# Kernel tuning notes

Hardware: AMD Instinct MI355X
Metric: run time of the kernel (lower is better)

Reference implementation:

```python
import math
import jax, jax.numpy as jnp
import numpy as np

B, T, C, H = 2, 1024, 1024, 16
D = C // H
BASE_SCALE = 0.03125
ATTN_ALPHA_INIT, MLP_ALPHA_INIT = 0.05, 0.05


def sinusoidal_embeddings(n, d):
    pos = jnp.arange(n, dtype=jnp.float32)[:, None]
    div = jnp.exp(jnp.arange(0, d, 2, dtype=jnp.float32) * (-math.log(10000.0) / d))
    emb = jnp.zeros((n, d), dtype=jnp.float32)
    emb = emb.at[:, 0::2].set(jnp.sin(pos * div))
    emb = emb.at[:, 1::2].set(jnp.cos(pos * div))
    return emb


def apply_rope(pos, q):
    # pos: (T, D); q: (B, H, T, D). Faithful to source: returns only the rotated-scaled component.
    pos = pos[-q.shape[2]:]
    d = q.shape[-1]
    sin, cos = pos[:, : d // 2], pos[:, d // 2 :]
    q_rot = jnp.stack((-q[..., 1::2], q[..., ::2]), axis=-1)  # (B,H,T,D/2,2)
    sc = jnp.stack((cos, sin), axis=-1)  # (T, D/2, 2)
    return (q_rot * sc).reshape(q.shape)


def justnorm(x):
    return x / jnp.linalg.norm(x, axis=-1, keepdims=True)


def setup_inputs() -> dict:
    key = jax.random.key(0)
    ks = jax.random.split(key, 14)
    w = lambda k, shape: jax.random.normal(k, shape, jnp.float32) * 0.02
    return {
        "h": jax.random.normal(ks[0], (B, T, C), jnp.float32),
        "Wq": w(ks[1], (C, C)),
        "Wk": w(ks[2], (C, C)),
        "Wv": w(ks[3], (C, C)),
        "Wo": w(ks[4], (C, C)),
        "Wfc": w(ks[5], (8 * C, C)),
        "Wproj": w(ks[6], (C, 4 * C)),
        "sqk": BASE_SCALE * jnp.ones(C) + w(ks[7], (C,)) * 0.05,
        "suv": jnp.ones(8 * C) + w(ks[8], (8 * C,)) * 0.05,
        "attn_alpha": BASE_SCALE * jnp.ones(C) + w(ks[9], (C,)) * 0.05,
        "mlp_alpha": BASE_SCALE * jnp.ones(C) + w(ks[10], (C,)) * 0.05,
        "thr_c": 1.6 * jnp.ones(H) + w(ks[11], (H,)) * 0.5,
        "stp": 10.0 * jnp.ones(H),
    }


def reference(h, Wq, Wk, Wv, Wo, Wfc, Wproj, sqk, suv, attn_alpha, mlp_alpha, thr_c, stp):
    softmax_scale = math.sqrt(D)  # nGPT uses sqrt(head_dim) since q,k are unit-normalized

    # --- attention branch (no pre-norm in nGPT mode) ---
    q = (h @ Wq.T).reshape(B, T, H, D).transpose(0, 2, 1, 3)  # (B,H,T,D)
    k = (h @ Wk.T).reshape(B, T, H, D).transpose(0, 2, 1, 3)
    v = (h @ Wv.T).reshape(B, T, H, D).transpose(0, 2, 1, 3)

    pos = sinusoidal_embeddings(T, D)
    q = apply_rope(pos, q)
    k = apply_rope(pos, k)

    sqk_s = (sqk * (1.0 / BASE_SCALE)).reshape(1, H, 1, D)
    q = sqk_s * justnorm(q)
    k = sqk_s * justnorm(k)

    scores = jnp.einsum("bhqd,bhkd->bhqk", q, k) * softmax_scale  # (B,H,T,T)
    causal = jnp.tril(jnp.ones((T, T), dtype=bool))
    w = jax.nn.softmax(jnp.where(causal, scores, -1e9), axis=-1)
    # soft score threshold: per-head sigmoid gate on raw scores, then renormalize
    gate = jax.nn.sigmoid(stp[None, :, None, None] * (scores - thr_c[None, :, None, None]))
    w = w * gate
    w = w / jnp.sum(w, axis=-1, keepdims=True)

    y = jnp.einsum("bhqk,bhkd->bhqd", w, v).transpose(0, 2, 1, 3).reshape(B, T, C)
    h_att = y @ Wo.T

    lr = jnp.abs(attn_alpha * (ATTN_ALPHA_INIT / BASE_SCALE))
    A = justnorm(h)
    Bn = justnorm(h_att)
    h = justnorm(A + lr * (Bn - A))

    # --- MLP branch ---
    uv = h @ Wfc.T  # (B,T,8C)
    uv = (suv * math.sqrt(C)) * uv
    u, vv = jnp.split(uv, 2, axis=-1)
    x_mlp = u * (vv * jax.nn.sigmoid(vv))
    h_mlp = x_mlp @ Wproj.T

    lr2 = jnp.abs(mlp_alpha * (MLP_ALPHA_INIT / BASE_SCALE))
    A = justnorm(h)
    Bn = justnorm(h_mlp)
    h = justnorm(A + lr2 * (Bn - A))
    return h
```

## Files before the change

### kernel.cpp

```cpp
#include <hip/hip_runtime.h>
#include <hip/hip_bf16.h>
#include <math.h>

typedef _Float16 f16x8 __attribute__((ext_vector_type(8)));
typedef float f32x4 __attribute__((ext_vector_type(4)));
typedef float f32x2 __attribute__((ext_vector_type(2)));
typedef unsigned short u16;
typedef unsigned int u32;
typedef u16 u16x4 __attribute__((ext_vector_type(4)));
typedef u16 u16x8 __attribute__((ext_vector_type(8)));

#define DEVI static __device__ __forceinline__
#define LDSS 72
#define MB (1u << 20)

DEVI u16 f2h(float f) {
    _Float16 h = (_Float16)f;
    return __builtin_bit_cast(u16, h);
}
DEVI float h2f(u16 u) {
    return (float)__builtin_bit_cast(_Float16, u);
}
DEVI f32x4 mfma16(f16x8 a, f16x8 b, f32x4 c) {
    return __builtin_amdgcn_mfma_f32_16x16x32_f16(a, b, c, 0, 0, 0);
}
DEVI void gload16(const u16* g, u16* l) {
    __builtin_amdgcn_global_load_lds((const __attribute__((address_space(1))) void*)g,
                                     (__attribute__((address_space(3))) void*)l, 16, 0, 0);
}

DEVI void stage128(const u16* __restrict__ g, size_t row0, int ldg, int k0, u16* lds) {
    int t = threadIdx.x;
    const u16* src = g + (row0 + (size_t)(t >> 3)) * (size_t)ldg + k0 + (t & 7) * 8;
    u16* dst = lds + (t >> 6) * 512;
#pragma unroll
    for (int is = 0; is < 4; is++)
        gload16(src + (size_t)is * 32 * ldg, dst + is * 2048);
}

DEVI void gemm128_core(const u16* __restrict__ A, const u16* __restrict__ B,
                       int ldk, int kbeg, int kend, int m0, int n0,
                       u16* As, u16* Bs, f32x4 acc[4][4]) {
    int lane = threadIdx.x & 63, w = threadIdx.x >> 6;
    int wm = (w >> 1) * 64, wn = (w & 1) * 64;
    int lrow = lane & 15, lg = lane >> 4;
    for (int k0 = kbeg; k0 < kend; k0 += 64) {
        __syncthreads();
        stage128(A, m0, ldk, k0, As);
        stage128(B, n0, ldk, k0, Bs);
        __syncthreads();
#pragma unroll
        for (int ks = 0; ks < 2; ks++) {
            f16x8 af[4], bf[4];
#pragma unroll
            for (int i = 0; i < 4; i++) {
                af[i] = *reinterpret_cast<f16x8*>(&As[(wm + i * 16 + lrow) * 64 + ks * 32 + lg * 8]);
                bf[i] = *reinterpret_cast<f16x8*>(&Bs[(wn + i * 16 + lrow) * 64 + ks * 32 + lg * 8]);
            }
#pragma unroll
            for (int i = 0; i < 4; i++)
#pragma unroll
                for (int j = 0; j < 4; j++)
                    acc[i][j] = mfma16(af[i], bf[j], acc[i][j]);
        }
    }
}

__global__ void cvt_kernel(const float* __restrict__ h, const float* __restrict__ Wq,
                           const float* __restrict__ Wk, const float* __restrict__ Wv,
                           const float* __restrict__ Wo, const float* __restrict__ Wfc,
                           const float* __restrict__ Wproj, u16* __restrict__ dst) {
    int bid = blockIdx.x;
    const float* src;
    size_t doff;
    int sb;
    if (bid < 1024)      { src = h;     sb = 0;    doff = 0; }
    else if (bid < 1536) { src = Wq;    sb = 1024; doff = 2097152; }
    else if (bid < 2048) { src = Wk;    sb = 1536; doff = 3145728; }
    else if (bid < 2560) { src = Wv;    sb = 2048; doff = 4194304; }
    else if (bid < 3072) { src = Wo;    sb = 2560; doff = 5242880; }
    else if (bid < 7168) { src = Wfc;   sb = 3072; doff = 10485760; }
    else                 { src = Wproj; sb = 7168; doff = 6291456; }
    size_t idx = (size_t)(bid - sb) * 2048 + threadIdx.x * 8;
    f32x4 a = *reinterpret_cast<const f32x4*>(src + idx);
    f32x4 b = *reinterpret_cast<const f32x4*>(src + idx + 4);
    u16x8 o;
    o[0] = f2h(a[0]); o[1] = f2h(a[1]); o[2] = f2h(a[2]); o[3] = f2h(a[3]);
    o[4] = f2h(b[0]); o[5] = f2h(b[1]); o[6] = f2h(b[2]); o[7] = f2h(b[3]);
    *reinterpret_cast<u16x8*>(dst + doff + idx) = o;
}

__global__ __launch_bounds__(256, 2) void qkv_h_kernel(
    const u16* __restrict__ hb, const u16* __restrict__ Wqh, const u16* __restrict__ Wkh,
    const u16* __restrict__ Wvh, u16* __restrict__ qb, u16* __restrict__ kb, u16* __restrict__ vb) {
    __shared__ u16 As[128 * 64];
    __shared__ u16 Bs[128 * 64];
    int z = blockIdx.z;
    const u16* W = (z == 0) ? Wqh : (z == 1) ? Wkh : Wvh;
    u16* dst = (z == 0) ? qb : (z == 1) ? kb : vb;
    int m0 = blockIdx.y * 128, n0 = blockIdx.x * 128;
    f32x4 acc[4][4];
    f32x4 zf = {0.f, 0.f, 0.f, 0.f};
#pragma unroll
    for (int i = 0; i < 4; i++)
#pragma unroll
        for (int j = 0; j < 4; j++) acc[i][j] = zf;
    gemm128_core(hb, W, 1024, 0, 1024, m0, n0, As, Bs, acc);
    int lane = threadIdx.x & 63, w = threadIdx.x >> 6;
    int wm = (w >> 1) * 64, wn = (w & 1) * 64;
    int lrow = lane & 15, lg = lane >> 4;
#pragma unroll
    for (int i = 0; i < 4; i++)
#pragma unroll
        for (int j = 0; j < 4; j++)
#pragma unroll
            for (int r = 0; r < 4; r++) {
                int m = m0 + wm + i * 16 + lg * 4 + r;
                int n = n0 + wn + j * 16 + lrow;
                dst[(size_t)m * 1024 + n] = f2h(acc[i][j][r]);
            }
}

__global__ __launch_bounds__(256, 2) void gemm_h_kernel(
    const u16* __restrict__ A, const u16* __restrict__ B, u16* __restrict__ out,
    int ldk, int ksplit, int osplit, int N) {
    __shared__ u16 As[128 * 64];
    __shared__ u16 Bs[128 * 64];
    int z = blockIdx.z;
    int m0 = blockIdx.y * 128, n0 = blockIdx.x * 128;
    f32x4 acc[4][4];
    f32x4 zf = {0.f, 0.f, 0.f, 0.f};
#pragma unroll
    for (int i = 0; i < 4; i++)
#pragma unroll
        for (int j = 0; j < 4; j++) acc[i][j] = zf;
    gemm128_core(A, B, ldk, z * ksplit, (z + 1) * ksplit, m0, n0, As, Bs, acc);
    u16* o = out + (size_t)z * osplit;
    int lane = threadIdx.x & 63, w = threadIdx.x >> 6;
    int wm = (w >> 1) * 64, wn = (w & 1) * 64;
    int lrow = lane & 15, lg = lane >> 4;
#pragma unroll
    for (int i = 0; i < 4; i++)
#pragma unroll
        for (int j = 0; j < 4; j++)
#pragma unroll
            for (int r = 0; r < 4; r++) {
                int m = m0 + wm + i * 16 + lg * 4 + r;
                int n = n0 + wn + j * 16 + lrow;
                o[(size_t)m * N + n] = f2h(acc[i][j][r]);
            }
}

__global__ void qkprep_kernel(u16* __restrict__ qb, u16* __restrict__ kb,
                              const float* __restrict__ sqk) {
    u16* buf = blockIdx.z ? kb : qb;
    int pair = blockIdx.x * 4 + (threadIdx.x >> 6);
    int m = pair >> 4, hh = pair & 15;
    int tt = m & 1023;
    int d = threadIdx.x & 63;
    size_t off = (size_t)m * 1024 + hh * 64 + d;
    float x = h2f(buf[off]);
    float xn = __shfl_xor(x, 1);
    int j = (d & 1) ? ((d - 1) >> 1) : (32 + (d >> 1));
    float dv = exp2f(-(float)(j >> 1) * 0.41524101186092029f);
    float ang = (float)tt * dv;
    float e = (j & 1) ? cosf(ang) : sinf(ang);
    float xr = (d & 1) ? (xn * e) : (-xn * e);
    float ss = xr * xr;
#pragma unroll
    for (int o = 1; o < 64; o <<= 1) ss += __shfl_xor(ss, o);
    float sc = rsqrtf(ss) * sqk[hh * 64 + d] * 32.0f;
    buf[off] = f2h(xr * sc);
}

__global__ __launch_bounds__(128) void attn_kernel(
    const u16* __restrict__ qb, const u16* __restrict__ kb, const u16* __restrict__ vb,
    const float* __restrict__ thr_c, const float* __restrict__ stp,
    u16* __restrict__ yph, f32x2* __restrict__ mden) {
    const int T = 1024, C = 1024;
    int qt = 31 - (blockIdx.x >> 2);
    int c = blockIdx.x & 3;
    int bh = blockIdx.y;
    int b = bh >> 4, hh = bh & 15;
    int q0 = qt * 32;
    int nkt = (q0 >> 6) + 1;
    __shared__ u16 Vt[2][64 * LDSS];
    __shared__ u16 Ps[32 * LDSS];
    int t = threadIdx.x;
    int lane = t & 63, w = t >> 6;
    int lrow = lane & 15, lg = lane >> 4, lk = lg * 8;
    int kvp = t & 31, db = t >> 5;

    const u16* qrowp = qb + (size_t)(b * T + q0 + w * 16 + lrow) * C + hh * 64;
    f16x8 qfr[2];
    qfr[0] = *reinterpret_cast<const f16x8*>(qrowp + lk);
    qfr[1] = *reinterpret_cast<const f16x8*>(qrowp + 32 + lk);

    float thr = thr_c[hh], st = stp[hh];
    float stthr = st * thr;
    float mrun = -1e30f, den = 0.f;
    f32x4 yacc[4];
    f32x4 zf = {0.f, 0.f, 0.f, 0.f};
#pragma unroll
    for (int i = 0; i < 4; i++) yacc[i] = zf;
    int qg = q0 + w * 16 + lrow;

    f16x8 kpre[8];
    u16x4 vr[8];
    const u16* kbase0 = kb + (size_t)(b * T + lrow) * C + hh * 64 + lk;
    const u16* vbase0 = vb + (size_t)(b * T + 2 * kvp) * C + hh * 64 + db * 16;

    if (c < nkt) {
        const u16* kbase = kbase0 + (size_t)(c << 6) * C;
        const u16* vsrc = vbase0 + (size_t)(c << 6) * C;
#pragma unroll
        for (int ks = 0; ks < 2; ks++)
#pragma unroll
            for (int f = 0; f < 4; f++)
                kpre[ks * 4 + f] = *reinterpret_cast<const f16x8*>(kbase + (size_t)(f * 16) * C + ks * 32);
#pragma unroll
        for (int dd = 0; dd < 4; dd++) {
            vr[dd * 2] = *reinterpret_cast<const u16x4*>(vsrc + dd * 4);
            vr[dd * 2 + 1] = *reinterpret_cast<const u16x4*>(vsrc + C + dd * 4);
        }
    }

    int bufsel = 0;
    for (int kt = c; kt < nkt; kt += 4) {
        int kv0 = kt << 6;
        u16* VB = Vt[bufsel];
        bufsel ^= 1;
#pragma unroll
        for (int dd = 0; dd < 4; dd++)
#pragma unroll
            for (int e = 0; e < 4; e++) {
                u32 v = (u32)vr[dd * 2][e] | ((u32)vr[dd * 2 + 1][e] << 16);
                *reinterpret_cast<u32*>(&VB[(db * 16 + dd * 4 + e) * LDSS + 2 * kvp]) = v;
            }
        f32x4 sacc[4];
#pragma unroll
        for (int f = 0; f < 4; f++) sacc[f] = zf;
        __builtin_amdgcn_s_setprio(1);
#pragma unroll
        for (int ks = 0; ks < 2; ks++)
#pragma unroll
            for (int f = 0; f < 4; f++)
                sacc[f] = mfma16(kpre[ks * 4 + f], qfr[ks], sacc[f]);
        __builtin_amdgcn_s_setprio(0);

        if (kt + 4 < nkt) {
            const u16* kbase = kbase0 + (size_t)((kt + 4) << 6) * C;
            const u16* vsrc = vbase0 + (size_t)((kt + 4) << 6) * C;
#pragma unroll
            for (int ks = 0; ks < 2; ks++)
#pragma unroll
                for (int f = 0; f < 4; f++)
                    kpre[ks * 4 + f] = *reinterpret_cast<const f16x8*>(kbase + (size_t)(f * 16) * C + ks * 32);
#pragma unroll
            for (int dd = 0; dd < 4; dd++) {
                vr[dd * 2] = *reinterpret_cast<const u16x4*>(vsrc + dd * 4);
                vr[dd * 2 + 1] = *reinterpret_cast<const u16x4*>(vsrc + C + dd * 4);
            }
        }

        float svv[16];
        float tmax = -1e30f;
        bool last = (kt == nkt - 1);
#pragma unroll
        for (int f = 0; f < 4; f++)
#pragma unroll
            for (int r = 0; r < 4; r++) {
                float s = sacc[f][r] * 8.0f;
                if (last) {
                    int kvg = kv0 + f * 16 + lg * 4 + r;
                    if (kvg > qg) s = -1e30f;
                }
                svv[f * 4 + r] = s;
                tmax = fmaxf(tmax, s);
            }
        tmax = fmaxf(tmax, __shfl_xor(tmax, 16));
        tmax = fmaxf(tmax, __shfl_xor(tmax, 32));
        float zM = stthr - st * tmax;
        float spM = tmax - __logf(1.0f + __expf(zM));
        float mnew = fmaxf(mrun, spM);
        float alpha = __expf(mrun - mnew);
        float tden = 0.f;
        u16 pu[16];
#pragma unroll
        for (int i = 0; i < 16; i++) {
            float s = svv[i];
            float e2 = __expf(s - mnew);
            float eg = __expf(stthr - st * s);
            float p = e2 * __builtin_amdgcn_rcpf(1.0f + eg);
            u16 ph = f2h(p);
            pu[i] = ph;
            tden += h2f(ph);
        }
        tden += __shfl_xor(tden, 16);
        tden += __shfl_xor(tden, 32);
        den = den * alpha + tden;
        mrun = mnew;

#pragma unroll
        for (int f = 0; f < 4; f++) {
            u16x4 u = {pu[f * 4 + 0], pu[f * 4 + 1], pu[f * 4 + 2], pu[f * 4 + 3]};
            *reinterpret_cast<u16x4*>(&Ps[(w * 16 + lrow) * LDSS + f * 16 + lg * 4]) = u;
        }
        float a4[4];
#pragma unroll
        for (int r = 0; r < 4; r++) a4[r] = __shfl(alpha, lg * 4 + r);
#pragma unroll
        for (int nf = 0; nf < 4; nf++)
#pragma unroll
            for (int r = 0; r < 4; r++) yacc[nf][r] *= a4[r];

        __syncthreads();

        __builtin_amdgcn_s_setprio(1);
#pragma unroll
        for (int ks = 0; ks < 2; ks++) {
            f16x8 pf = *reinterpret_cast<f16x8*>(&Ps[(w * 16 + lrow) * LDSS + ks * 32 + lk]);
#pragma unroll
            for (int nf = 0; nf < 4; nf++) {
                f16x8 vf = *reinterpret_cast<f16x8*>(&VB[(nf * 16 + lrow) * LDSS + ks * 32 + lk]);
                yacc[nf] = mfma16(pf, vf, yacc[nf]);
            }
        }
        __builtin_amdgcn_s_setprio(0);
    }
    u16* ypc = yph + (size_t)c * 2097152;
#pragma unroll
    for (int nf = 0; nf < 4; nf++)
#pragma unroll
        for (int r = 0; r < 4; r++) {
            int qrow = q0 + w * 16 + lg * 4 + r;
            ypc[(size_t)(b * T + qrow) * C + hh * 64 + nf * 16 + lrow] = f2h(yacc[nf][r]);
        }
    if (lg == 0) {
        f32x2 md;
        md[0] = mrun; md[1] = den;
        mden[((size_t)c * 32 + bh) * 1024 + (q0 + w * 16 + lrow)] = md;
    }
}

__global__ void attn_merge_kernel(const u16* __restrict__ yph, const f32x2* __restrict__ mden,
                                  u16* __restrict__ y) {
    int row = blockIdx.x;
    int b = row >> 10, tr = row & 1023;
    int t = threadIdx.x;
#pragma unroll
    for (int i = 0; i < 4; i++) {
        int idx = t + 256 * i;
        int hh = idx >> 6;
        float m[4], d[4];
        float M = -1e30f;
#pragma unroll
        for (int p = 0; p < 4; p++) {
            f32x2 md = mden[((size_t)p * 32 + b * 16 + hh) * 1024 + tr];
            m[p] = md[0]; d[p] = md[1];
            M = fmaxf(M, m[p]);
        }
        size_t off = (size_t)row * 1024 + idx;
        float dn = 0.f, acc = 0.f;
#pragma unroll
        for (int p = 0; p < 4; p++) {
            float wp = __expf(m[p] - M);
            dn += d[p] * wp;
            acc += h2f(yph[off + (size_t)p * 2097152]) * wp;
        }
        y[off] = f2h(acc / dn);
    }
}

__global__ __launch_bounds__(256, 2) void fc_silu_kernel(
    const u16* __restrict__ h1h, const u16* __restrict__ Wfch,
    const float* __restrict__ suv, u16* __restrict__ xmlp) {
    __shared__ u16 As[128 * 64];
    __shared__ u16 Bu[128 * 64];
    __shared__ u16 Bv[128 * 64];
    int m0 = blockIdx.y * 128, n0 = blockIdx.x * 128;
    f32x4 au[4][4], av[4][4];
    f32x4 zf = {0.f, 0.f, 0.f, 0.f};
#pragma unroll
    for (int i = 0; i < 4; i++)
#pragma unroll
        for (int j = 0; j < 4; j++) { au[i][j] = zf; av[i][j] = zf; }
    int lane = threadIdx.x & 63, w = threadIdx.x >> 6;
    int wm = (w >> 1) * 64, wn = (w & 1) * 64;
    int lrow = lane & 15, lg = lane >> 4;
    for (int k0 = 0; k0 < 1024; k0 += 64) {
        __syncthreads();
        stage128(h1h, m0, 1024, k0, As);
        stage128(Wfch, n0, 1024, k0, Bu);
        stage128(Wfch, 4096 + n0, 1024, k0, Bv);
        __syncthreads();
#pragma unroll
        for (int ks = 0; ks < 2; ks++) {
            f16x8 af[4], bu[4], bv[4];
#pragma unroll
            for (int i = 0; i < 4; i++) {
                af[i] = *reinterpret_cast<f16x8*>(&As[(wm + i * 16 + lrow) * 64 + ks * 32 + lg * 8]);
                bu[i] = *reinterpret_cast<f16x8*>(&Bu[(wn + i * 16 + lrow) * 64 + ks * 32 + lg * 8]);
                bv[i] = *reinterpret_cast<f16x8*>(&Bv[(wn + i * 16 + lrow) * 64 + ks * 32 + lg * 8]);
            }
#pragma unroll
            for (int i = 0; i < 4; i++)
#pragma unroll
                for (int j = 0; j < 4; j++) {
                    au[i][j] = mfma16(af[i], bu[j], au[i][j]);
                    av[i][j] = mfma16(af[i], bv[j], av[i][j]);
                }
        }
    }
#pragma unroll
    for (int i = 0; i < 4; i++)
#pragma unroll
        for (int j = 0; j < 4; j++) {
            int n = n0 + wn + j * 16 + lrow;
            float su = suv[n] * 32.0f;
            float sv = suv[4096 + n] * 32.0f;
#pragma unroll
            for (int r = 0; r < 4; r++) {
                int m = m0 + wm + i * 16 + lg * 4 + r;
                float uu = au[i][j][r] * su;
                float vv = av[i][j][r] * sv;
                float sig = 1.0f / (1.0f + __expf(-vv));
                xmlp[(size_t)m * 4096 + n] = f2h(uu * vv * sig);
            }
        }
}

__global__ void normres_kernel(const float* __restrict__ base, const u16* __restrict__ dparts,
                               int nparts, int pstride, const float* __restrict__ alpha,
                               float* __restrict__ outf, u16* __restrict__ outh) {
    int row = blockIdx.x;
    int t = threadIdx.x;
    const float* pb = base + (size_t)row * 1024;
    float xb[4], xd[4];
    float ssb = 0.f, ssd = 0.f;
#pragma unroll
    for (int i = 0; i < 4; i++) {
        size_t off = (size_t)row * 1024 + t + 256 * i;
        xb[i] = pb[t + 256 * i];
        float d = 0.f;
        for (int p = 0; p < nparts; p++) d += h2f(dparts[off + (size_t)p * pstride]);
        xd[i] = d;
        ssb += xb[i] * xb[i];
        ssd += xd[i] * xd[i];
    }
#pragma unroll
    for (int o = 1; o < 64; o <<= 1) { ssb += __shfl_xor(ssb, o); ssd += __shfl_xor(ssd, o); }
    __shared__ float red[8];
    int w = t >> 6;
    if ((t & 63) == 0) { red[w * 2] = ssb; red[w * 2 + 1] = ssd; }
    __syncthreads();
    ssb = red[0] + red[2] + red[4] + red[6];
    ssd = red[1] + red[3] + red[5] + red[7];
    float rb = rsqrtf(ssb), rd = rsqrtf(ssd);
    float c[4];
    float ssc = 0.f;
#pragma unroll
    for (int i = 0; i < 4; i++) {
        float a = xb[i] * rb;
        float bb = xd[i] * rd;
        float lr = fabsf(alpha[t + 256 * i] * 1.6f);
        float cv = a + lr * (bb - a);
        c[i] = cv;
        ssc += cv * cv;
    }
#pragma unroll
    for (int o = 1; o < 64; o <<= 1) ssc += __shfl_xor(ssc, o);
    __syncthreads();
    if ((t & 63) == 0) red[w] = ssc;
    __syncthreads();
    ssc = red[0] + red[1] + red[2] + red[3];
    float rc = rsqrtf(ssc);
#pragma unroll
    for (int i = 0; i < 4; i++) {
        float v = c[i] * rc;
        size_t off = (size_t)row * 1024 + t + 256 * i;
        outf[off] = v;
        if (outh) outh[off] = f2h(v);
    }
}

extern "C" void kernel_launch(void* const* d_in, const int* in_sizes, int n_in,
                              void* d_out, int out_size, void* d_ws, size_t ws_size,
                              hipStream_t stream) {
    const float* h = (const float*)d_in[0];
    const float* Wq = (const float*)d_in[1];
    const float* Wk = (const float*)d_in[2];
    const float* Wv = (const float*)d_in[3];
    const float* Wo = (const float*)d_in[4];
    const float* Wfc = (const float*)d_in[5];
    const float* Wproj = (const float*)d_in[6];
    const float* sqk = (const float*)d_in[7];
    const float* suv = (const float*)d_in[8];
    const float* attn_alpha = (const float*)d_in[9];
    const float* mlp_alpha = (const float*)d_in[10];
    const float* thr_c = (const float*)d_in[11];
    const float* stp = (const float*)d_in[12];

    char* ws = (char*)d_ws;
    u16* f16heap = (u16*)ws;
    u16* hb     = f16heap + 0;
    u16* Wqh    = f16heap + 2097152;
    u16* Wkh    = f16heap + 3145728;
    u16* Wvh    = f16heap + 4194304;
    u16* Woh    = f16heap + 5242880;
    u16* Wprojh = f16heap + 6291456;
    u16* Wfch   = f16heap + 10485760;
    u16* partsP = Wfch;
    u16* qb   = (u16*)(ws + (size_t)36 * MB);
    u16* kb   = (u16*)(ws + (size_t)40 * MB);
    u16* vb   = (u16*)(ws + (size_t)44 * MB);
    u16* y    = (u16*)(ws + (size_t)48 * MB);
    u16* yph  = (u16*)(ws + (size_t)52 * MB);
    f32x2* mden = (f32x2*)(ws + (size_t)68 * MB);
    u16* hattP = (u16*)(ws + (size_t)52 * MB);
    float* h1 = (float*)(ws + (size_t)36 * MB);
    u16* h1h  = (u16*)(ws + (size_t)44 * MB);
    u16* xmlp = (u16*)(ws + (size_t)52 * MB);
    float* out = (float*)d_out;

    cvt_kernel<<<9216, 256, 0, stream>>>(h, Wq, Wk, Wv, Wo, Wfc, Wproj, f16heap);
    qkv_h_kernel<<<dim3(8, 16, 3), 256, 0, stream>>>(hb, Wqh, Wkh, Wvh, qb, kb, vb);
    qkprep_kernel<<<dim3(8192, 1, 2), 256, 0, stream>>>(qb, kb, sqk);
    attn_kernel<<<dim3(128, 32), 128, 0, stream>>>(qb, kb, vb, thr_c, stp, yph, mden);
    attn_merge_kernel<<<2048, 256, 0, stream>>>(yph, mden, y);
    gemm_h_kernel<<<dim3(8, 16, 4), 256, 0, stream>>>(y, Woh, hattP, 1024, 256, 2097152, 1024);
    normres_kernel<<<2048, 256, 0, stream>>>(h, hattP, 4, 2097152, attn_alpha, h1, h1h);
    fc_silu_kernel<<<dim3(32, 16), 256, 0, stream>>>(h1h, Wfch, suv, xmlp);
    gemm_h_kernel<<<dim3(8, 16, 4), 256, 0, stream>>>(xmlp, Wprojh, partsP, 4096, 1024, 2097152, 1024);
    normres_kernel<<<2048, 256, 0, stream>>>(h1, partsP, 4, 2097152, mlp_alpha, out, (u16*)nullptr);
}
```

Before: 204.0 us.

## Enlarge attention query tile to 64 rows with four waves per block

The attention kernel now processes 64 query rows per block using 256 threads (four waves) instead of 32 rows with two waves, halving the grid. Each K/V tile loaded into registers and LDS is now shared by twice as many query rows, and each thread stages half as much V data, cutting global K/V traffic per query. In exchange there are fewer blocks and coarser causal granularity, which lowers parallelism and can waste work on the diagonal tile.

```diff
diff --git a/kernel.cpp b/kernel.cpp
--- a/kernel.cpp
+++ b/kernel.cpp
@@ -173,25 +173,25 @@
     buf[off] = f2h(xr * sc);
 }
 
-__global__ __launch_bounds__(128) void attn_kernel(
+__global__ __launch_bounds__(256) void attn_kernel(
     const u16* __restrict__ qb, const u16* __restrict__ kb, const u16* __restrict__ vb,
     const float* __restrict__ thr_c, const float* __restrict__ stp,
     u16* __restrict__ yph, f32x2* __restrict__ mden) {
     const int T = 1024, C = 1024;
-    int qt = 31 - (blockIdx.x >> 2);
+    int p = 15 - (blockIdx.x >> 2);
     int c = blockIdx.x & 3;
     int bh = blockIdx.y;
     int b = bh >> 4, hh = bh & 15;
-    int q0 = qt * 32;
-    int nkt = (q0 >> 6) + 1;
+    int nkt = p + 1;
     __shared__ u16 Vt[2][64 * LDSS];
-    __shared__ u16 Ps[32 * LDSS];
+    __shared__ u16 Ps[64 * LDSS];
     int t = threadIdx.x;
     int lane = t & 63, w = t >> 6;
     int lrow = lane & 15, lg = lane >> 4, lk = lg * 8;
     int kvp = t & 31, db = t >> 5;
 
-    const u16* qrowp = qb + (size_t)(b * T + q0 + w * 16 + lrow) * C + hh * 64;
+    int qrow0 = 64 * p + 16 * w;
+    const u16* qrowp = qb + (size_t)(b * T + qrow0 + lrow) * C + hh * 64;
     f16x8 qfr[2];
     qfr[0] = *reinterpret_cast<const f16x8*>(qrowp + lk);
     qfr[1] = *reinterpret_cast<const f16x8*>(qrowp + 32 + lk);
@@ -203,12 +203,12 @@
     f32x4 zf = {0.f, 0.f, 0.f, 0.f};
 #pragma unroll
     for (int i = 0; i < 4; i++) yacc[i] = zf;
-    int qg = q0 + w * 16 + lrow;
+    int qg = qrow0 + lrow;
 
     f16x8 kpre[8];
-    u16x4 vr[8];
+    u16x4 vr[4];
     const u16* kbase0 = kb + (size_t)(b * T + lrow) * C + hh * 64 + lk;
-    const u16* vbase0 = vb + (size_t)(b * T + 2 * kvp) * C + hh * 64 + db * 16;
+    const u16* vbase0 = vb + (size_t)(b * T + 2 * kvp) * C + hh * 64 + db * 8;
 
     if (c < nkt) {
         const u16* kbase = kbase0 + (size_t)(c << 6) * C;
@@ -218,11 +218,10 @@
 #pragma unroll
             for (int f = 0; f < 4; f++)
                 kpre[ks * 4 + f] = *reinterpret_cast<const f16x8*>(kbase + (size_t)(f * 16) * C + ks * 32);
-#pragma unroll
-        for (int dd = 0; dd < 4; dd++) {
-            vr[dd * 2] = *reinterpret_cast<const u16x4*>(vsrc + dd * 4);
-            vr[dd * 2 + 1] = *reinterpret_cast<const u16x4*>(vsrc + C + dd * 4);
-        }
+        vr[0] = *reinterpret_cast<const u16x4*>(vsrc);
+        vr[1] = *reinterpret_cast<const u16x4*>(vsrc + 4);
+        vr[2] = *reinterpret_cast<const u16x4*>(vsrc + C);
+        vr[3] = *reinterpret_cast<const u16x4*>(vsrc + C + 4);
     }
 
     int bufsel = 0;
@@ -231,11 +230,11 @@
         u16* VB = Vt[bufsel];
         bufsel ^= 1;
 #pragma unroll
-        for (int dd = 0; dd < 4; dd++)
+        for (int dd = 0; dd < 2; dd++)
 #pragma unroll
             for (int e = 0; e < 4; e++) {
-                u32 v = (u32)vr[dd * 2][e] | ((u32)vr[dd * 2 + 1][e] << 16);
-                *reinterpret_cast<u32*>(&VB[(db * 16 + dd * 4 + e) * LDSS + 2 * kvp]) = v;
+                u32 v = (u32)vr[dd][e] | ((u32)vr[2 + dd][e] << 16);
+                *reinterpret_cast<u32*>(&VB[(db * 8 + dd * 4 + e) * LDSS + 2 * kvp]) = v;
             }
         f32x4 sacc[4];
 #pragma unroll
@@ -256,11 +255,10 @@
 #pragma unroll
                 for (int f = 0; f < 4; f++)
                     kpre[ks * 4 + f] = *reinterpret_cast<const f16x8*>(kbase + (size_t)(f * 16) * C + ks * 32);
-#pragma unroll
-            for (int dd = 0; dd < 4; dd++) {
-                vr[dd * 2] = *reinterpret_cast<const u16x4*>(vsrc + dd * 4);
-                vr[dd * 2 + 1] = *reinterpret_cast<const u16x4*>(vsrc + C + dd * 4);
-            }
+            vr[0] = *reinterpret_cast<const u16x4*>(vsrc);
+            vr[1] = *reinterpret_cast<const u16x4*>(vsrc + 4);
+            vr[2] = *reinterpret_cast<const u16x4*>(vsrc + C);
+            vr[3] = *reinterpret_cast<const u16x4*>(vsrc + C + 4);
         }
 
         float svv[16];
@@ -291,8 +289,8 @@
             float s = svv[i];
             float e2 = __expf(s - mnew);
             float eg = __expf(stthr - st * s);
-            float p = e2 * __builtin_amdgcn_rcpf(1.0f + eg);
-            u16 ph = f2h(p);
+            float pp = e2 * __builtin_amdgcn_rcpf(1.0f + eg);
+            u16 ph = f2h(pp);
             pu[i] = ph;
             tden += h2f(ph);
         }
@@ -333,13 +331,13 @@
     for (int nf = 0; nf < 4; nf++)
 #pragma unroll
         for (int r = 0; r < 4; r++) {
-            int qrow = q0 + w * 16 + lg * 4 + r;
+            int qrow = qrow0 + lg * 4 + r;
             ypc[(size_t)(b * T + qrow) * C + hh * 64 + nf * 16 + lrow] = f2h(yacc[nf][r]);
         }
     if (lg == 0) {
         f32x2 md;
         md[0] = mrun; md[1] = den;
-        mden[((size_t)c * 32 + bh) * 1024 + (q0 + w * 16 + lrow)] = md;
+        mden[((size_t)c * 32 + bh) * 1024 + (qrow0 + lrow)] = md;
     }
 }
 
@@ -526,7 +524,7 @@
     cvt_kernel<<<9216, 256, 0, stream>>>(h, Wq, Wk, Wv, Wo, Wfc, Wproj, f16heap);
     qkv_h_kernel<<<dim3(8, 16, 3), 256, 0, stream>>>(hb, Wqh, Wkh, Wvh, qb, kb, vb);
     qkprep_kernel<<<dim3(8192, 1, 2), 256, 0, stream>>>(qb, kb, sqk);
-    attn_kernel<<<dim3(128, 32), 128, 0, stream>>>(qb, kb, vb, thr_c, stp, yph, mden);
+    attn_kernel<<<dim3(64, 32), 256, 0, stream>>>(qb, kb, vb, thr_c, stp, yph, mden);
     attn_merge_kernel<<<2048, 256, 0, stream>>>(yph, mden, y);
     gemm_h_kernel<<<dim3(8, 16, 4), 256, 0, stream>>>(y, Woh, hattP, 1024, 256, 2097152, 1024);
     normres_kernel<<<2048, 256, 0, stream>>>(h, hattP, 4, 2097152, attn_alpha, h1, h1h);
```

Measured after the change: 204.6 us. No clear change (+0.3%).
